# Optimization experiments

Measured on AMD Instinct MI355X. Metric: run time of the kernel, lower is better.

Reference implementation:

```python
import jax, jax.numpy as jnp
import numpy as np

L = 3          # num_legs
D = 32         # leg_dim == out_leg_dim (output_dim = input_dim = D**L)
NUM_NODES = 6  # num_levels * (num_legs - 1) = 3 * 2
B = 256        # batch


def setup_inputs() -> dict:
    key = jax.random.key(0)
    k1, k2 = jax.random.split(key, 2)
    inputs = jax.random.normal(k1, (B, D ** L), dtype=jnp.float32)
    # all 6 entangler nodes share shape (D,D,D,D) since leg_dim == out_leg_dim;
    # scale ~ 1/D to mimic glorot and keep the 6-contraction chain numerically sane
    nodes = jax.random.normal(k2, (NUM_NODES, D, D, D, D), dtype=jnp.float32) / D
    bias = jnp.zeros((D ** L,), dtype=jnp.float32)
    return {"inputs": inputs, "nodes": nodes, "bias": bias}


def reference(inputs, nodes, bias):
    # Faithful port of DenseEntangler.call: reshape the input vector to L legs,
    # then contract NUM_NODES 4-leg tensors; node i eats edge slots (i%L, (i+1)%L)
    # with its axes (0,1) and replaces them with its axes (2,3).
    # jnp.tensordot output axis order (free axes of x in order, then node axes 2,3)
    # matches tn.contract_between's default ordering, so the final flatten is identical.
    Bn = inputs.shape[0]
    x = inputs.reshape((Bn,) + (D,) * L)   # axis 0 = batch, axes 1..L = legs
    pos = list(range(1, L + 1))            # edge slot k -> current axis of x
    for i in range(NUM_NODES):
        s0, s1 = i % L, (i + 1) % L
        p, q = pos[s0], pos[s1]
        x = jnp.tensordot(x, nodes[i], axes=[[p, q], [0, 1]])
        # remaining axes of x keep order (batch stays axis 0); new node axes go last
        new_pos = [0] * L
        for k in range(L):
            if k == s0:
                new_pos[k] = L - 1
            elif k == s1:
                new_pos[k] = L
            else:
                a = pos[k]
                new_pos[k] = a - (p < a) - (q < a)
        pos = new_pos
    out = x.reshape(Bn, -1) + bias  # flatten in current axis order, as in the TF code
    return jax.nn.relu(out)
```

## Files before the change

### kernel.cpp

```cpp
#include <hip/hip_runtime.h>
#include <hip/hip_bf16.h>
#include <stdint.h>

using bf16 = __hip_bfloat16;
typedef __attribute__((ext_vector_type(8))) short short8;
typedef __attribute__((ext_vector_type(4))) float floatx4;

#define DD 32
#define DL3 32768
#define BATCH 256
#define NK 1024
#define LDS_BYTES 131072

__device__ __forceinline__ int swz(int b) {
  return b ^ ((((b) >> 7) & 3) << 4) ^ ((((b) >> 13) & 3) << 5);
}

__global__ __launch_bounds__(256) void prep_nodes(const float* __restrict__ nodes, bf16* __restrict__ dst) {
  int id = blockIdx.x;
  int nb = id & 31, kb = (id >> 5) & 31, i = id >> 10;
  const float* src = nodes + (size_t)i * 1048576;
  bf16* d = dst + (size_t)i * 1048576;
  __shared__ float tile[32][33];
  int t = threadIdx.x;
#pragma unroll
  for (int it = 0; it < 4; ++it) {
    int u = (t >> 5) + it * 8, j = t & 31;
    tile[u][j] = src[(size_t)(u * 32 + kb) * 1024 + nb * 32 + j];
  }
  __syncthreads();
#pragma unroll
  for (int it = 0; it < 4; ++it) {
    int j = (t >> 5) + it * 8, u = t & 31;
    d[(size_t)(nb * 32 + j) * 1024 + kb * 32 + u] = __float2bfloat16(tile[u][j]);
  }
}

__global__ __launch_bounds__(256) void prep_frag(const bf16* __restrict__ nodeT, bf16* __restrict__ nodeTf) {
  int id = blockIdx.x;
  int kc = id & 31, i = id >> 5;
  const bf16* src = nodeT + (size_t)i * 1048576 + kc * 32;
  bf16* dst = nodeTf + (size_t)i * 1048576 + (size_t)kc * 32768;
  int t = threadIdx.x;
#pragma unroll
  for (int it = 0; it < 16; ++it) {
    int o = it * 256 + t;
    int lane = o & 63, nt = o >> 6;
    int n = nt * 16 + (lane & 15), q = lane >> 4;
    short8 vv = *(const short8*)(src + (size_t)n * 1024 + q * 8);
    *(short8*)(dst + (size_t)o * 8) = vv;
  }
}

#define LDB(buf, kc_) { const char* _p = Bs + (size_t)(kc_) * 65536;          \
  _Pragma("unroll") for (int _j = 0; _j < 8; ++_j)                            \
    buf[_j] = *(const short8*)(_p + _j * 1024); }

#define LDA(af_, kc_) { _Pragma("unroll") for (int _i = 0; _i < 2; ++_i) {    \
  int _a = aLow[_i] + (kc_) * 2048; _a ^= ((_a >> 13) & 3) << 5;              \
  af_[_i] = *(const short8*)(sIn + _a); } }

#define MM(buf, af_) { _Pragma("unroll") for (int _i = 0; _i < 2; ++_i)       \
  _Pragma("unroll") for (int _j = 0; _j < 8; ++_j)                            \
    acc[_i][_j] = __builtin_amdgcn_mfma_f32_16x16x32_bf16(af_[_i], buf[_j], acc[_i][_j], 0, 0, 0); }

#define BODY_L(kc_, buf, nbuf) { LDB(nbuf, (kc_) + 3);                        \
  short8 _af[2]; LDA(_af, kc_); MM(buf, _af); }
#define BODY_N(kc_, buf) { short8 _af[2]; LDA(_af, kc_); MM(buf, _af); }

__global__ __launch_bounds__(512, 2) void entangler_batch(
    const float* __restrict__ x, const bf16* __restrict__ nodeTf,
    float* __restrict__ out, const float* __restrict__ bias) {
  extern __shared__ char smem[];
  char* st0 = smem;
  char* st1 = smem + 65536;

  const int t = threadIdx.x;
  const int lane = t & 63;
  const int lane16 = lane & 15, quad = lane >> 4;
  const int w = t >> 6;
  const int b = blockIdx.x;

  const float* xb = x + (size_t)b * DL3;
#pragma unroll
  for (int it = 0; it < 16; ++it) {
    int flat = it * 512 + t;
    floatx4 vx = *(const floatx4*)(xb + flat * 4);
    int e0 = flat * 4;
    int f = e0 & 31, v = (e0 >> 5) & 31, u = e0 >> 10;
#pragma unroll
    for (int e = 0; e < 4; ++e) {
      int byte = v * 2048 + (f + e) * 64 + u * 2;
      *(bf16*)(st0 + swz(byte)) = __float2bfloat16(vx[e]);
    }
  }

  int aLow[2];
#pragma unroll
  for (int i2 = 0; i2 < 2; ++i2) {
    int bb = (i2 * 16 + lane16) * 64 + quad * 16;
    aLow[i2] = bb ^ (((bb >> 7) & 3) << 4);
  }

  const char* Bb = (const char*)nodeTf + (size_t)((w * 8) * 512 + lane * 8) * 2;

  char* sIn = st0;
  char* sOut = st1;
  __syncthreads();

#pragma unroll 1
  for (int s = 0; s < 6; ++s) {
    const char* Bs = Bb + (size_t)s * 2097152;

    floatx4 acc[2][8];
#pragma unroll
    for (int i2 = 0; i2 < 2; ++i2)
#pragma unroll
      for (int j = 0; j < 8; ++j)
        acc[i2][j] = (floatx4){0.f, 0.f, 0.f, 0.f};

    short8 bb0[8], bb1[8], bb2[8], bb3[8];
    LDB(bb0, 0); LDB(bb1, 1); LDB(bb2, 2);
#pragma unroll 1
    for (int kc0 = 0; kc0 < 28; kc0 += 4) {
      BODY_L(kc0 + 0, bb0, bb3);
      BODY_L(kc0 + 1, bb1, bb0);
      BODY_L(kc0 + 2, bb2, bb1);
      BODY_L(kc0 + 3, bb3, bb2);
    }
    BODY_L(28, bb0, bb3);
    BODY_N(29, bb1);
    BODY_N(30, bb2);
    BODY_N(31, bb3);

    if (s < 5) {
#pragma unroll
      for (int i2 = 0; i2 < 2; ++i2) {
#pragma unroll
        for (int j = 0; j < 8; ++j) {
#pragma unroll
          for (int r = 0; r < 4; ++r) {
            int f = i2 * 16 + quad * 4 + r;
            int n = w * 128 + j * 16 + lane16;
            int byte = f * 2048 + n * 2;
            *(bf16*)(sOut + swz(byte)) = __float2bfloat16(acc[i2][j][r]);
          }
        }
      }
      __syncthreads();
      char* tmp = sIn; sIn = sOut; sOut = tmp;
    } else {
      float* ob = out + (size_t)b * DL3;
#pragma unroll
      for (int i2 = 0; i2 < 2; ++i2) {
#pragma unroll
        for (int j = 0; j < 8; ++j) {
#pragma unroll
          for (int r = 0; r < 4; ++r) {
            int f = i2 * 16 + quad * 4 + r;
            int n = w * 128 + j * 16 + lane16;
            float v = acc[i2][j][r] + bias[f * 1024 + n];
            ob[f * 1024 + n] = fmaxf(v, 0.f);
          }
        }
      }
    }
  }
}

extern "C" void kernel_launch(void* const* d_in, const int* in_sizes, int n_in,
                              void* d_out, int out_size, void* d_ws, size_t ws_size,
                              hipStream_t stream) {
  const float* x     = (const float*)d_in[0];
  const float* nodes = (const float*)d_in[1];
  const float* bias  = (const float*)d_in[2];
  float* out = (float*)d_out;

  bf16* nodeT  = (bf16*)d_ws;
  bf16* nodeTf = nodeT + (size_t)6 * 1048576;

  static bool attr_done = false;
  if (!attr_done) {
    hipFuncSetAttribute((const void*)entangler_batch,
                        hipFuncAttributeMaxDynamicSharedMemorySize, LDS_BYTES);
    attr_done = true;
  }

  prep_nodes<<<dim3(6 * 1024), dim3(256), 0, stream>>>(nodes, nodeT);
  prep_frag<<<dim3(6 * 32), dim3(256), 0, stream>>>(nodeT, nodeTf);
  entangler_batch<<<dim3(BATCH), dim3(512), LDS_BYTES, stream>>>(x, nodeTf, out, bias);
}
```

Before: 255.7 us.

## Fuse node prep into one kernel and split GEMM across 16 waves per block

Merges the two node-preparation kernels into a single kernel that reads fp32 nodes, converts them to bf16 and writes the MFMA fragment layout through LDS, removing the intermediate transposed buffer and one launch. The main kernel now uses 1024 threads (16 waves), each computing a 32x64 tile instead of 32x128. B-fragment prefetch depth drops from three stages to a simple double buffer. The goal is more waves to hide latency and fewer registers per thread. The cost is less B reuse per wave and a shallower prefetch, and 128 KB of LDS per block still limits residency to one block per CU.

```diff
diff --git a/kernel.cpp b/kernel.cpp
--- a/kernel.cpp
+++ b/kernel.cpp
@@ -6,54 +6,54 @@
 typedef __attribute__((ext_vector_type(8))) short short8;
 typedef __attribute__((ext_vector_type(4))) float floatx4;
 
-#define DD 32
 #define DL3 32768
 #define BATCH 256
-#define NK 1024
 #define LDS_BYTES 131072
 
 __device__ __forceinline__ int swz(int b) {
   return b ^ ((((b) >> 7) & 3) << 4) ^ ((((b) >> 13) & 3) << 5);
 }
 
-__global__ __launch_bounds__(256) void prep_nodes(const float* __restrict__ nodes, bf16* __restrict__ dst) {
-  int id = blockIdx.x;
-  int nb = id & 31, kb = (id >> 5) & 31, i = id >> 10;
-  const float* src = nodes + (size_t)i * 1048576;
-  bf16* d = dst + (size_t)i * 1048576;
-  __shared__ float tile[32][33];
-  int t = threadIdx.x;
-#pragma unroll
-  for (int it = 0; it < 4; ++it) {
-    int u = (t >> 5) + it * 8, j = t & 31;
-    tile[u][j] = src[(size_t)(u * 32 + kb) * 1024 + nb * 32 + j];
-  }
-  __syncthreads();
-#pragma unroll
-  for (int it = 0; it < 4; ++it) {
-    int j = (t >> 5) + it * 8, u = t & 31;
-    d[(size_t)(nb * 32 + j) * 1024 + kb * 32 + u] = __float2bfloat16(tile[u][j]);
-  }
-}
-
-__global__ __launch_bounds__(256) void prep_frag(const bf16* __restrict__ nodeT, bf16* __restrict__ nodeTf) {
+__global__ __launch_bounds__(256) void prep_frag2(const float* __restrict__ nodes,
+                                                  bf16* __restrict__ nodeTf) {
   int id = blockIdx.x;
   int kc = id & 31, i = id >> 5;
-  const bf16* src = nodeT + (size_t)i * 1048576 + kc * 32;
+  __shared__ bf16 sb[32][514];
+  const float* base = nodes + (size_t)i * 1048576 + (size_t)kc * 1024;
   bf16* dst = nodeTf + (size_t)i * 1048576 + (size_t)kc * 32768;
   int t = threadIdx.x;
+#pragma unroll 1
+  for (int np = 0; np < 2; ++np) {
 #pragma unroll
-  for (int it = 0; it < 16; ++it) {
-    int o = it * 256 + t;
-    int lane = o & 63, nt = o >> 6;
-    int n = nt * 16 + (lane & 15), q = lane >> 4;
-    short8 vv = *(const short8*)(src + (size_t)n * 1024 + q * 8);
-    *(short8*)(dst + (size_t)o * 8) = vv;
+    for (int c = 0; c < 16; ++c) {
+      int g4 = c * 256 + t;
+      int u = g4 >> 7, c4 = g4 & 127;
+      floatx4 v4 = *(const floatx4*)(base + (size_t)u * 32768 + np * 512 + c4 * 4);
+      bf16* row = &sb[u][c4 * 4];
+      row[0] = __float2bfloat16(v4[0]);
+      row[1] = __float2bfloat16(v4[1]);
+      row[2] = __float2bfloat16(v4[2]);
+      row[3] = __float2bfloat16(v4[3]);
+    }
+    __syncthreads();
+#pragma unroll
+    for (int c = 0; c < 8; ++c) {
+      int g = c * 256 + t;
+      int lane = g & 63, ntl = g >> 6;
+      int l16 = lane & 15, q = lane >> 4;
+      short8 vv;
+#pragma unroll
+      for (int e = 0; e < 8; ++e)
+        vv[e] = *(const short*)&sb[q * 8 + e][ntl * 16 + l16];
+      int nt = np * 32 + ntl;
+      *(short8*)(dst + (size_t)nt * 512 + lane * 8) = vv;
+    }
+    __syncthreads();
   }
 }
 
 #define LDB(buf, kc_) { const char* _p = Bs + (size_t)(kc_) * 65536;          \
-  _Pragma("unroll") for (int _j = 0; _j < 8; ++_j)                            \
+  _Pragma("unroll") for (int _j = 0; _j < 4; ++_j)                            \
     buf[_j] = *(const short8*)(_p + _j * 1024); }
 
 #define LDA(af_, kc_) { _Pragma("unroll") for (int _i = 0; _i < 2; ++_i) {    \
@@ -61,14 +61,10 @@
   af_[_i] = *(const short8*)(sIn + _a); } }
 
 #define MM(buf, af_) { _Pragma("unroll") for (int _i = 0; _i < 2; ++_i)       \
-  _Pragma("unroll") for (int _j = 0; _j < 8; ++_j)                            \
+  _Pragma("unroll") for (int _j = 0; _j < 4; ++_j)                            \
     acc[_i][_j] = __builtin_amdgcn_mfma_f32_16x16x32_bf16(af_[_i], buf[_j], acc[_i][_j], 0, 0, 0); }
 
-#define BODY_L(kc_, buf, nbuf) { LDB(nbuf, (kc_) + 3);                        \
-  short8 _af[2]; LDA(_af, kc_); MM(buf, _af); }
-#define BODY_N(kc_, buf) { short8 _af[2]; LDA(_af, kc_); MM(buf, _af); }
-
-__global__ __launch_bounds__(512, 2) void entangler_batch(
+__global__ __launch_bounds__(1024, 4) void entangler_batch(
     const float* __restrict__ x, const bf16* __restrict__ nodeTf,
     float* __restrict__ out, const float* __restrict__ bias) {
   extern __shared__ char smem[];
@@ -83,8 +79,8 @@
 
   const float* xb = x + (size_t)b * DL3;
 #pragma unroll
-  for (int it = 0; it < 16; ++it) {
-    int flat = it * 512 + t;
+  for (int it = 0; it < 8; ++it) {
+    int flat = it * 1024 + t;
     floatx4 vx = *(const floatx4*)(xb + flat * 4);
     int e0 = flat * 4;
     int f = e0 & 31, v = (e0 >> 5) & 31, u = e0 >> 10;
@@ -102,7 +98,7 @@
     aLow[i2] = bb ^ (((bb >> 7) & 3) << 4);
   }
 
-  const char* Bb = (const char*)nodeTf + (size_t)((w * 8) * 512 + lane * 8) * 2;
+  const char* Bb = (const char*)nodeTf + (size_t)(w * 4096) + (size_t)(lane * 16);
 
   char* sIn = st0;
   char* sOut = st1;
@@ -112,36 +108,34 @@
   for (int s = 0; s < 6; ++s) {
     const char* Bs = Bb + (size_t)s * 2097152;
 
-    floatx4 acc[2][8];
+    floatx4 acc[2][4];
 #pragma unroll
     for (int i2 = 0; i2 < 2; ++i2)
 #pragma unroll
-      for (int j = 0; j < 8; ++j)
+      for (int j = 0; j < 4; ++j)
         acc[i2][j] = (floatx4){0.f, 0.f, 0.f, 0.f};
 
-    short8 bb0[8], bb1[8], bb2[8], bb3[8];
-    LDB(bb0, 0); LDB(bb1, 1); LDB(bb2, 2);
+    short8 b0[4], b1[4], afE[2], afO[2];
+    LDB(b0, 0);
 #pragma unroll 1
-    for (int kc0 = 0; kc0 < 28; kc0 += 4) {
-      BODY_L(kc0 + 0, bb0, bb3);
-      BODY_L(kc0 + 1, bb1, bb0);
-      BODY_L(kc0 + 2, bb2, bb1);
-      BODY_L(kc0 + 3, bb3, bb2);
+    for (int kc = 0; kc < 32; kc += 2) {
+      LDB(b1, kc + 1);
+      LDA(afE, kc);
+      MM(b0, afE);
+      if (kc + 2 < 32) LDB(b0, kc + 2);
+      LDA(afO, kc + 1);
+      MM(b1, afO);
     }
-    BODY_L(28, bb0, bb3);
-    BODY_N(29, bb1);
-    BODY_N(30, bb2);
-    BODY_N(31, bb3);
 
     if (s < 5) {
 #pragma unroll
       for (int i2 = 0; i2 < 2; ++i2) {
 #pragma unroll
-        for (int j = 0; j < 8; ++j) {
+        for (int j = 0; j < 4; ++j) {
 #pragma unroll
           for (int r = 0; r < 4; ++r) {
             int f = i2 * 16 + quad * 4 + r;
-            int n = w * 128 + j * 16 + lane16;
+            int n = w * 64 + j * 16 + lane16;
             int byte = f * 2048 + n * 2;
             *(bf16*)(sOut + swz(byte)) = __float2bfloat16(acc[i2][j][r]);
           }
@@ -154,11 +148,11 @@
 #pragma unroll
       for (int i2 = 0; i2 < 2; ++i2) {
 #pragma unroll
-        for (int j = 0; j < 8; ++j) {
+        for (int j = 0; j < 4; ++j) {
 #pragma unroll
           for (int r = 0; r < 4; ++r) {
             int f = i2 * 16 + quad * 4 + r;
-            int n = w * 128 + j * 16 + lane16;
+            int n = w * 64 + j * 16 + lane16;
             float v = acc[i2][j][r] + bias[f * 1024 + n];
             ob[f * 1024 + n] = fmaxf(v, 0.f);
           }
@@ -176,8 +170,7 @@
   const float* bias  = (const float*)d_in[2];
   float* out = (float*)d_out;
 
-  bf16* nodeT  = (bf16*)d_ws;
-  bf16* nodeTf = nodeT + (size_t)6 * 1048576;
+  bf16* nodeTf = (bf16*)d_ws;
 
   static bool attr_done = false;
   if (!attr_done) {
@@ -186,7 +179,6 @@
     attr_done = true;
   }
 
-  prep_nodes<<<dim3(6 * 1024), dim3(256), 0, stream>>>(nodes, nodeT);
-  prep_frag<<<dim3(6 * 32), dim3(256), 0, stream>>>(nodeT, nodeTf);
-  entangler_batch<<<dim3(BATCH), dim3(512), LDS_BYTES, stream>>>(x, nodeTf, out, bias);
+  prep_frag2<<<dim3(6 * 32), dim3(256), 0, stream>>>(nodes, nodeTf);
+  entangler_batch<<<dim3(BATCH), dim3(1024), LDS_BYTES, stream>>>(x, nodeTf, out, bias);
 }
```

New measurement: 307.5 us. 20.2% more time.
